# Kernel tuning notes

Hardware: AMD Instinct MI355X
Metric: run time of the kernel (lower is better)

The kernel has to match this reference:

```python
import jax, jax.numpy as jnp
import numpy as np


def _conv_relu(x, w, b):
    # keras Conv2D: NHWC input, HWIO kernel, VALID padding, stride 1, relu
    y = jax.lax.conv_general_dilated(
        x, w, window_strides=(1, 1), padding='VALID',
        dimension_numbers=('NHWC', 'HWIO', 'NHWC'))
    return jax.nn.relu(y + b)


def _maxpool2(x):
    # keras MaxPooling2D((2,2)): window 2x2, stride 2, VALID
    return jax.lax.reduce_window(
        x, -jnp.inf, jax.lax.max,
        window_dimensions=(1, 2, 2, 1), window_strides=(1, 2, 2, 1),
        padding='VALID')


def setup_inputs() -> dict:
    key = jax.random.key(0)
    ks = jax.random.split(key, 8)
    B = 4096
    return {
        'x': jax.random.normal(ks[0], (B, 14, 14, 1), jnp.float32),
        'conv1_w': jax.random.normal(ks[1], (3, 3, 1, 32), jnp.float32) * 0.1,
        'conv1_b': jnp.zeros((32,), jnp.float32),
        'conv2_w': jax.random.normal(ks[2], (3, 3, 32, 64), jnp.float32) * 0.05,
        'conv2_b': jnp.zeros((64,), jnp.float32),
        # trainable grid, initialized as tf.linspace(0,1,grid_size=50)
        'grid': jnp.linspace(0.0, 1.0, 50, dtype=jnp.float32),
        # KANLayer splines: output_dim=128 weights, each (input_dim=256, grid_size=50)
        'kan1_w': jax.random.normal(ks[3], (128, 256, 50), jnp.float32) * 0.05,
        # SimplifiedKANLayer splines: output_dim=64 weights, each (input_dim=128,)
        'kan2_w': jax.random.normal(ks[4], (64, 128), jnp.float32) * 0.05,
        'dense_w': jax.random.normal(ks[5], (64, 10), jnp.float32) * 0.05,
        'dense_b': jnp.zeros((10,), jnp.float32),
    }


def reference(x, conv1_w, conv1_b, conv2_w, conv2_b, grid, kan1_w, kan2_w,
              dense_w, dense_b):
    h = _conv_relu(x, conv1_w, conv1_b)   # (B,12,12,32)
    h = _maxpool2(h)                      # (B,6,6,32)
    h = _conv_relu(h, conv2_w, conv2_b)   # (B,4,4,64)
    h = _maxpool2(h)                      # (B,2,2,64)
    B = h.shape[0]
    h = h.reshape(B, -1)                  # (B,256) keras Flatten order (H,W,C)
    # KANLayer: linear hat basis relu(1-|x-g|) per (feature,grid), contracted
    # against per-output coefficients: out[b,o] = sum_{d,g} W[o,d,g]*basis[b,d,g]
    basis = jax.nn.relu(1.0 - jnp.abs(h[:, :, None] - grid[None, None, :]))  # (B,256,50)
    h = jnp.einsum('bdg,odg->bo', basis, kan1_w)  # (B,128)
    # SimplifiedKANLayer: out[b,o] = sum_d W2[o,d]*relu(h[b,d])
    h = jnp.einsum('bd,od->bo', jax.nn.relu(h), kan2_w)  # (B,64)
    return jax.nn.softmax(h @ dense_w + dense_b, axis=-1)  # (B,10)
```

## Files before the change

kernel.cpp:

```cpp
#include <hip/hip_runtime.h>
#include <hip/hip_bf16.h>
#include <hip/hip_fp16.h>

typedef float v2f __attribute__((ext_vector_type(2)));
typedef _Float16 f16x8 __attribute__((ext_vector_type(8)));
typedef float f32x4 __attribute__((ext_vector_type(4)));

__global__ __launch_bounds__(256) void k_prep(
    const float* __restrict__ kan1_w, const float* __restrict__ w2,
    const float* __restrict__ kan2_w, __half* __restrict__ tabN,
    _Float16* __restrict__ w2f, __half2* __restrict__ w2t) {
  int bid = blockIdx.x;
  int t = threadIdx.x;
  if (bid < 256) {
    if (t < 128) {
      int d = bid, o = t;
      const float* wp = kan1_w + (size_t)o * 12800 + (size_t)d * 50;
      float w[50];
#pragma unroll
      for (int i = 0; i < 25; ++i) {
        float2 v = *(const float2*)(wp + 2 * i);
        w[2 * i] = v.x;
        w[2 * i + 1] = v.y;
      }
      float lowW = w[0], lowG = 0.f;
      float highW = 0.f, highG = 0.f;
#pragma unroll
      for (int g = 1; g < 50; ++g) {
        highW += w[g];
        highG += w[g] * ((float)g * (1.0f / 49.0f));
      }
      __half* trow = tabN + (size_t)d * 197 * 128 + o;
      const float inv98 = 1.0f / 98.0f;
#pragma unroll
      for (int j = 0; j < 98; ++j) {
        float A = highW - lowW;
        float Bc = (lowW + highW) + lowG - highG;
        float c0 = (float)(2 * j) * inv98 + 0.5f * inv98;
        float c1 = c0 + inv98;
        trow[(size_t)(2 * j) * 128] = __float2half(fmaf(A, c0, Bc));
        trow[(size_t)(2 * j + 1) * 128] = __float2half(fmaf(A, c1, Bc));
        if (j + 1 <= 49) {
          float wg = w[j + 1], gg = (float)(j + 1) * (1.0f / 49.0f);
          lowW += wg; lowG += wg * gg;
          highW -= wg; highG -= wg * gg;
        }
        if (j >= 48) {
          float wg = w[j - 48], gg = (float)(j - 48) * (1.0f / 49.0f);
          lowW -= wg; lowG -= wg * gg;
        }
      }
      trow[(size_t)196 * 128] = __float2half(0.f);
    }
    return;
  }
  if (bid < 328) {
    int i = (bid - 256) * 256 + t;
    int n = i & 63;
    int row = i >> 6;
    int ci = row & 31;
    int tap = row >> 5;
    w2f[((tap * 4 + (ci >> 3)) * 64 + n) * 8 + (ci & 7)] = (_Float16)w2[i];
    return;
  }
  {
    int i = (bid - 328) * 256 + t;
    int dp = i >> 6;
    int o = i & 63;
    w2t[i] = __floats2half2_rn(kan2_w[o * 128 + 2 * dp],
                               kan2_w[o * 128 + 2 * dp + 1]);
  }
}

#define NBC 4

__global__ __launch_bounds__(256) void k_main(
    const float* __restrict__ x, const float* __restrict__ w1,
    const float* __restrict__ b1, const _Float16* __restrict__ w2f,
    const float* __restrict__ b2, const __half* __restrict__ tabN,
    const __half2* __restrict__ w2t, const float* __restrict__ dense_w,
    const float* __restrict__ dense_b, float* __restrict__ out) {
  __shared__ __align__(16) char sm1[4864];
  __shared__ __align__(16) char sm2[11520];
  float* xs = (float*)sm1;
  float* w1s = xs + NBC * 224;
  float* b1s = w1s + 288;
  unsigned short* meta = (unsigned short*)sm1;
  _Float16* h1l = (_Float16*)sm2;
  float* vs = (float*)sm2;
  float* us = vs + NBC * 128;
  float* ls = us + NBC * 64;
  int t = threadIdx.x;
  int bid = blockIdx.x;
  int b0 = bid * NBC;
  {
    for (int i = t; i < NBC * 224; i += 256) {
      int blb = i / 224;
      int rem = i - blb * 224;
      int r = rem >> 4;
      int cc = rem & 15;
      xs[i] = (cc < 14) ? x[(size_t)(b0 + blb) * 196 + r * 14 + cc] : 0.f;
    }
    for (int i = t; i < 288; i += 256) w1s[i] = w1[i];
    if (t < 32) b1s[t] = b1[t];
  }
  __syncthreads();
  int p = t >> 6;
  int c = t & 63;
  {
    int ch = c & 31;
    int half = c >> 5;
    float wr[9];
#pragma unroll
    for (int j = 0; j < 9; ++j) wr[j] = w1s[j * 32 + ch];
    float bias = b1s[ch];
    int y0 = 3 * half;
    const float* xb = xs + p * 224;
    _Float16* hrow = h1l + p * 1440 + ch;
#pragma unroll
    for (int yy = 0; yy < 3; ++yy) {
      int y = y0 + yy;
      float xr[4][16];
#pragma unroll
      for (int r = 0; r < 4; ++r) {
        float4* dstp = (float4*)xr[r];
        const float4* srcp = (const float4*)(xb + (2 * y + r) * 16);
#pragma unroll
        for (int q = 0; q < 4; ++q) dstp[q] = srcp[q];
      }
#pragma unroll
      for (int xx = 0; xx < 6; ++xx) {
        float m = -1e30f;
#pragma unroll
        for (int py = 0; py < 2; ++py)
#pragma unroll
          for (int px = 0; px < 2; ++px) {
            float s = 0.f;
#pragma unroll
            for (int dy = 0; dy < 3; ++dy)
#pragma unroll
              for (int dx = 0; dx < 3; ++dx)
                s = fmaf(xr[py + dy][2 * xx + px + dx], wr[dy * 3 + dx], s);
            m = fmaxf(m, s);
          }
        hrow[(y * 6 + xx) * 40] = (_Float16)fmaxf(m + bias, 0.f);
      }
    }
  }
  __syncthreads();
  {
    int lm = c & 15;
    int lk = c >> 4;
    int mbase = (lm >> 2) * 6 + (lm & 3);
    f32x4 acc[4];
#pragma unroll
    for (int nt = 0; nt < 4; ++nt) acc[nt] = (f32x4){0.f, 0.f, 0.f, 0.f};
    const _Float16* h0 = &h1l[p * 1440 + lk * 8];
#pragma unroll
    for (int tap = 0; tap < 9; ++tap) {
      int tapoff = (tap / 3) * 6 + (tap % 3);
      int po = (mbase + tapoff) * 40;
      f16x8 a0 = *(const f16x8*)(h0 + po);
      const _Float16* wb = &w2f[((tap * 4 + lk) * 64 + lm) * 8];
      f16x8 bf0 = *(const f16x8*)(wb);
      f16x8 bf1 = *(const f16x8*)(wb + 128);
      f16x8 bf2 = *(const f16x8*)(wb + 256);
      f16x8 bf3 = *(const f16x8*)(wb + 384);
      acc[0] = __builtin_amdgcn_mfma_f32_16x16x32_f16(a0, bf0, acc[0], 0, 0, 0);
      acc[1] = __builtin_amdgcn_mfma_f32_16x16x32_f16(a0, bf1, acc[1], 0, 0, 0);
      acc[2] = __builtin_amdgcn_mfma_f32_16x16x32_f16(a0, bf2, acc[2], 0, 0, 0);
      acc[3] = __builtin_amdgcn_mfma_f32_16x16x32_f16(a0, bf3, acc[3], 0, 0, 0);
    }
    float bias[4];
#pragma unroll
    for (int nt = 0; nt < 4; ++nt) bias[nt] = b2[nt * 16 + lm];
#pragma unroll
    for (int nt = 0; nt < 4; ++nt) {
      f32x4 A = acc[nt];
      float m01 = fmaxf(A.x, A.y);
      float m23 = fmaxf(A.z, A.w);
      m01 = fmaxf(m01, __shfl_xor(m01, 16));
      m23 = fmaxf(m23, __shfl_xor(m23, 16));
      float val = (lk & 1) ? m23 : m01;
      val = fmaxf(val + bias[nt], 0.f);
      int d = lk * 64 + nt * 16 + lm;
      int k = (int)(val * 98.0f);
      k = k > 196 ? 196 : k;
      meta[d * NBC + p] = (unsigned short)(d * 197 + k);
    }
  }
  __syncthreads();
  {
    int lq = c >> 4;
    int lo = c & 15;
    int phase0 = bid & 7;
    v2f acc[4];
#pragma unroll
    for (int e = 0; e < 4; ++e) acc[e] = (v2f){0.f, 0.f};
    for (int ph = 0; ph < 8; ++ph) {
      int d0 = ((phase0 + ph) & 7) << 5;
      int offs[8];
#pragma unroll
      for (int dq = 0; dq < 8; ++dq)
        offs[dq] = ((int)meta[(d0 + 4 * dq + lq) * NBC + p]) << 7;
      float4 raws[8];
#pragma unroll
      for (int dq = 0; dq < 8; ++dq)
        raws[dq] = *(const float4*)(tabN + offs[dq] + lo * 8);
#pragma unroll
      for (int dq = 0; dq < 8; ++dq) {
        float2 f0 = __half22float2(__builtin_bit_cast(__half2, raws[dq].x));
        float2 f1 = __half22float2(__builtin_bit_cast(__half2, raws[dq].y));
        float2 f2 = __half22float2(__builtin_bit_cast(__half2, raws[dq].z));
        float2 f3 = __half22float2(__builtin_bit_cast(__half2, raws[dq].w));
        acc[0] += (v2f){f0.x, f0.y};
        acc[1] += (v2f){f1.x, f1.y};
        acc[2] += (v2f){f2.x, f2.y};
        acc[3] += (v2f){f3.x, f3.y};
      }
    }
#pragma unroll
    for (int e = 0; e < 4; ++e) {
      acc[e].x += __shfl_xor(acc[e].x, 16);
      acc[e].y += __shfl_xor(acc[e].y, 16);
      acc[e].x += __shfl_xor(acc[e].x, 32);
      acc[e].y += __shfl_xor(acc[e].y, 32);
    }
    if (lq == 0) {
      float* vp = vs + p * 128 + lo * 8;
      *(float4*)vp = make_float4(fmaxf(acc[0].x, 0.f), fmaxf(acc[0].y, 0.f),
                                 fmaxf(acc[1].x, 0.f), fmaxf(acc[1].y, 0.f));
      *(float4*)(vp + 4) =
          make_float4(fmaxf(acc[2].x, 0.f), fmaxf(acc[2].y, 0.f),
                      fmaxf(acc[3].x, 0.f), fmaxf(acc[3].y, 0.f));
    }
  }
  __syncthreads();
  {
    float a = 0.f;
    const float* v0 = vs + p * 128;
#pragma unroll 8
    for (int dp = 0; dp < 64; ++dp) {
      float2 wf = __half22float2(w2t[dp * 64 + c]);
      float2 vq = *(const float2*)(v0 + 2 * dp);
      a = fmaf(wf.x, vq.x, a);
      a = fmaf(wf.y, vq.y, a);
    }
    us[p * 64 + c] = a;
  }
  __syncthreads();
  if (t < NBC * 10) {
    int b = t / 10;
    int j = t - b * 10;
    float s = dense_b[j];
    for (int k2 = 0; k2 < 64; ++k2)
      s = fmaf(us[b * 64 + k2], dense_w[k2 * 10 + j], s);
    ls[b * 12 + j] = s;
  }
  __syncthreads();
  if (t < NBC) {
    int b = t;
    float m = -1e30f;
#pragma unroll
    for (int j = 0; j < 10; ++j) m = fmaxf(m, ls[b * 12 + j]);
    float e[10];
    float sum = 0.f;
#pragma unroll
    for (int j = 0; j < 10; ++j) {
      e[j] = __expf(ls[b * 12 + j] - m);
      sum += e[j];
    }
    float inv = 1.0f / sum;
#pragma unroll
    for (int j = 0; j < 10; ++j) out[(size_t)(b0 + b) * 10 + j] = e[j] * inv;
  }
}

extern "C" void kernel_launch(void* const* d_in, const int* in_sizes, int n_in,
                              void* d_out, int out_size, void* d_ws, size_t ws_size,
                              hipStream_t stream) {
  const float* x      = (const float*)d_in[0];
  const float* w1     = (const float*)d_in[1];
  const float* b1     = (const float*)d_in[2];
  const float* w2     = (const float*)d_in[3];
  const float* b2     = (const float*)d_in[4];
  const float* kan1_w = (const float*)d_in[6];
  const float* kan2_w = (const float*)d_in[7];
  const float* dw     = (const float*)d_in[8];
  const float* db     = (const float*)d_in[9];
  float* out = (float*)d_out;
  int B = in_sizes[0] / 196;

  char* wsb = (char*)d_ws;
  __half* tabN = (__half*)wsb;
  size_t off1 = (size_t)256 * 197 * 128 * sizeof(__half);
  off1 = (off1 + 255) & ~(size_t)255;
  _Float16* w2f = (_Float16*)(wsb + off1);
  size_t off2 = off1 + 18432 * sizeof(_Float16);
  off2 = (off2 + 255) & ~(size_t)255;
  __half2* w2t = (__half2*)(wsb + off2);

  k_prep<<<dim3(344), dim3(256), 0, stream>>>(kan1_w, w2, kan2_w, tabN, w2f, w2t);
  k_main<<<dim3(B / NBC), dim3(256), 0, stream>>>(
      x, w1, b1, w2f, b2, tabN, w2t, dw, db, out);
}
```

Baseline: 112.5 us.

## Double main kernel threads and split prep table build across all threads

k_main now runs 512 threads per block. The extra four waves split the conv1 output columns and the KAN gather over the feature dimension, then combine their partial sums in the second KAN layer. k_prep stages kan1_w rows through shared memory and splits the 98-step table build between two thread halves, so all 256 threads work instead of 128. The aim is more waves in flight to hide gather latency, paid for with extra LDS traffic, partial-sum merging, and conv2 running on only half the waves.

```diff
diff --git a/kernel.cpp b/kernel.cpp
--- a/kernel.cpp
+++ b/kernel.cpp
@@ -10,48 +10,57 @@
     const float* __restrict__ kan1_w, const float* __restrict__ w2,
     const float* __restrict__ kan2_w, __half* __restrict__ tabN,
     _Float16* __restrict__ w2f, __half2* __restrict__ w2t) {
+  __shared__ float wsh[128][51];
   int bid = blockIdx.x;
   int t = threadIdx.x;
   if (bid < 256) {
-    if (t < 128) {
-      int d = bid, o = t;
-      const float* wp = kan1_w + (size_t)o * 12800 + (size_t)d * 50;
-      float w[50];
-#pragma unroll
-      for (int i = 0; i < 25; ++i) {
-        float2 v = *(const float2*)(wp + 2 * i);
-        w[2 * i] = v.x;
-        w[2 * i + 1] = v.y;
-      }
-      float lowW = w[0], lowG = 0.f;
-      float highW = 0.f, highG = 0.f;
-#pragma unroll
+    int d = bid;
+    for (int i = t; i < 128 * 50; i += 256) {
+      int oo = i / 50;
+      int g = i - oo * 50;
+      wsh[oo][g] = kan1_w[(size_t)oo * 12800 + (size_t)d * 50 + g];
+    }
+    __syncthreads();
+    int o = t & 127;
+    int jh = t >> 7;
+    const float* wr = &wsh[o][0];
+    __half* trow = tabN + (size_t)d * 197 * 128 + o;
+    const float inv98 = 1.0f / 98.0f;
+    float lowW, lowG, highW, highG;
+    int k0, k1;
+    if (jh == 0) {
+      lowW = wr[0]; lowG = 0.f; highW = 0.f; highG = 0.f;
       for (int g = 1; g < 50; ++g) {
-        highW += w[g];
-        highG += w[g] * ((float)g * (1.0f / 49.0f));
-      }
-      __half* trow = tabN + (size_t)d * 197 * 128 + o;
-      const float inv98 = 1.0f / 98.0f;
-#pragma unroll
-      for (int j = 0; j < 98; ++j) {
-        float A = highW - lowW;
-        float Bc = (lowW + highW) + lowG - highG;
-        float c0 = (float)(2 * j) * inv98 + 0.5f * inv98;
-        float c1 = c0 + inv98;
-        trow[(size_t)(2 * j) * 128] = __float2half(fmaf(A, c0, Bc));
-        trow[(size_t)(2 * j + 1) * 128] = __float2half(fmaf(A, c1, Bc));
-        if (j + 1 <= 49) {
-          float wg = w[j + 1], gg = (float)(j + 1) * (1.0f / 49.0f);
-          lowW += wg; lowG += wg * gg;
-          highW -= wg; highG -= wg * gg;
-        }
-        if (j >= 48) {
-          float wg = w[j - 48], gg = (float)(j - 48) * (1.0f / 49.0f);
-          lowW -= wg; lowG -= wg * gg;
-        }
-      }
-      trow[(size_t)196 * 128] = __float2half(0.f);
-    }
+        highW += wr[g];
+        highG += wr[g] * ((float)g * (1.0f / 49.0f));
+      }
+      k0 = 0; k1 = 49;
+    } else {
+      lowW = 0.f; lowG = 0.f; highW = 0.f; highG = 0.f;
+      for (int g = 1; g < 50; ++g) {
+        lowW += wr[g];
+        lowG += wr[g] * ((float)g * (1.0f / 49.0f));
+      }
+      k0 = 49; k1 = 98;
+    }
+    for (int k = k0; k < k1; ++k) {
+      float A = highW - lowW;
+      float Bc = (lowW + highW) + lowG - highG;
+      float c0 = (float)(2 * k) * inv98 + 0.5f * inv98;
+      float c1 = c0 + inv98;
+      trow[(size_t)(2 * k) * 128] = __float2half(fmaf(A, c0, Bc));
+      trow[(size_t)(2 * k + 1) * 128] = __float2half(fmaf(A, c1, Bc));
+      if (k + 1 <= 49) {
+        float wg = wr[k + 1], gg = (float)(k + 1) * (1.0f / 49.0f);
+        lowW += wg; lowG += wg * gg;
+        highW -= wg; highG -= wg * gg;
+      }
+      if (k >= 48) {
+        float wg = wr[k - 48], gg = (float)(k - 48) * (1.0f / 49.0f);
+        lowW -= wg; lowG -= wg * gg;
+      }
+    }
+    if (jh == 1) trow[(size_t)196 * 128] = __float2half(0.f);
     return;
   }
   if (bid < 328) {
@@ -74,7 +83,7 @@
 
 #define NBC 4
 
-__global__ __launch_bounds__(256) void k_main(
+__global__ __launch_bounds__(512) void k_main(
     const float* __restrict__ x, const float* __restrict__ w1,
     const float* __restrict__ b1, const _Float16* __restrict__ w2f,
     const float* __restrict__ b2, const __half* __restrict__ tabN,
@@ -88,33 +97,36 @@
   unsigned short* meta = (unsigned short*)sm1;
   _Float16* h1l = (_Float16*)sm2;
   float* vs = (float*)sm2;
-  float* us = vs + NBC * 128;
-  float* ls = us + NBC * 64;
+  float* us = (float*)(sm2 + 4096);
+  float* ls = (float*)(sm2 + 6144);
   int t = threadIdx.x;
   int bid = blockIdx.x;
   int b0 = bid * NBC;
-  {
-    for (int i = t; i < NBC * 224; i += 256) {
+  int w = t >> 6;
+  int c = t & 63;
+  int p = w & 3;
+  int half = w >> 2;
+  {
+    for (int i = t; i < NBC * 224; i += 512) {
       int blb = i / 224;
       int rem = i - blb * 224;
       int r = rem >> 4;
       int cc = rem & 15;
       xs[i] = (cc < 14) ? x[(size_t)(b0 + blb) * 196 + r * 14 + cc] : 0.f;
     }
-    for (int i = t; i < 288; i += 256) w1s[i] = w1[i];
-    if (t < 32) b1s[t] = b1[t];
-  }
-  __syncthreads();
-  int p = t >> 6;
-  int c = t & 63;
+    if (t < 288) w1s[t] = w1[t];
+    else if (t < 320) b1s[t - 288] = b1[t - 288];
+  }
+  __syncthreads();
   {
     int ch = c & 31;
-    int half = c >> 5;
+    int yh = c >> 5;
     float wr[9];
 #pragma unroll
     for (int j = 0; j < 9; ++j) wr[j] = w1s[j * 32 + ch];
     float bias = b1s[ch];
-    int y0 = 3 * half;
+    int y0 = 3 * yh;
+    int x0 = 3 * half;
     const float* xb = xs + p * 224;
     _Float16* hrow = h1l + p * 1440 + ch;
 #pragma unroll
@@ -129,7 +141,8 @@
         for (int q = 0; q < 4; ++q) dstp[q] = srcp[q];
       }
 #pragma unroll
-      for (int xx = 0; xx < 6; ++xx) {
+      for (int xx = 0; xx < 3; ++xx) {
+        int xc = x0 + xx;
         float m = -1e30f;
 #pragma unroll
         for (int py = 0; py < 2; ++py)
@@ -140,15 +153,15 @@
             for (int dy = 0; dy < 3; ++dy)
 #pragma unroll
               for (int dx = 0; dx < 3; ++dx)
-                s = fmaf(xr[py + dy][2 * xx + px + dx], wr[dy * 3 + dx], s);
+                s = fmaf(xr[py + dy][2 * xc + px + dx], wr[dy * 3 + dx], s);
             m = fmaxf(m, s);
           }
-        hrow[(y * 6 + xx) * 40] = (_Float16)fmaxf(m + bias, 0.f);
-      }
-    }
-  }
-  __syncthreads();
-  {
+        hrow[(y * 6 + xc) * 40] = (_Float16)fmaxf(m + bias, 0.f);
+      }
+    }
+  }
+  __syncthreads();
+  if (half == 0) {
     int lm = c & 15;
     int lk = c >> 4;
     int mbase = (lm >> 2) * 6 + (lm & 3);
@@ -193,12 +206,13 @@
   {
     int lq = c >> 4;
     int lo = c & 15;
-    int phase0 = bid & 7;
+    int dbase = half << 7;
+    int phase0 = bid & 3;
     v2f acc[4];
 #pragma unroll
     for (int e = 0; e < 4; ++e) acc[e] = (v2f){0.f, 0.f};
-    for (int ph = 0; ph < 8; ++ph) {
-      int d0 = ((phase0 + ph) & 7) << 5;
+    for (int ph = 0; ph < 4; ++ph) {
+      int d0 = dbase + (((phase0 + ph) & 3) << 5);
       int offs[8];
 #pragma unroll
       for (int dq = 0; dq < 8; ++dq)
@@ -227,26 +241,29 @@
       acc[e].y += __shfl_xor(acc[e].y, 32);
     }
     if (lq == 0) {
-      float* vp = vs + p * 128 + lo * 8;
-      *(float4*)vp = make_float4(fmaxf(acc[0].x, 0.f), fmaxf(acc[0].y, 0.f),
-                                 fmaxf(acc[1].x, 0.f), fmaxf(acc[1].y, 0.f));
-      *(float4*)(vp + 4) =
-          make_float4(fmaxf(acc[2].x, 0.f), fmaxf(acc[2].y, 0.f),
-                      fmaxf(acc[3].x, 0.f), fmaxf(acc[3].y, 0.f));
+      float* vp = vs + (half * NBC + p) * 128 + lo * 8;
+      *(float4*)vp = make_float4(acc[0].x, acc[0].y, acc[1].x, acc[1].y);
+      *(float4*)(vp + 4) = make_float4(acc[2].x, acc[2].y, acc[3].x, acc[3].y);
     }
   }
   __syncthreads();
   {
     float a = 0.f;
     const float* v0 = vs + p * 128;
+    const float* v1 = vs + (NBC + p) * 128;
+    int dp0 = half * 32;
 #pragma unroll 8
-    for (int dp = 0; dp < 64; ++dp) {
+    for (int dpi = 0; dpi < 32; ++dpi) {
+      int dp = dp0 + dpi;
       float2 wf = __half22float2(w2t[dp * 64 + c]);
-      float2 vq = *(const float2*)(v0 + 2 * dp);
-      a = fmaf(wf.x, vq.x, a);
-      a = fmaf(wf.y, vq.y, a);
-    }
-    us[p * 64 + c] = a;
+      float2 qa = *(const float2*)(v0 + 2 * dp);
+      float2 qb = *(const float2*)(v1 + 2 * dp);
+      float vx = fmaxf(qa.x + qb.x, 0.f);
+      float vy = fmaxf(qa.y + qb.y, 0.f);
+      a = fmaf(wf.x, vx, a);
+      a = fmaf(wf.y, vy, a);
+    }
+    us[(half * NBC + p) * 64 + c] = a;
   }
   __syncthreads();
   if (t < NBC * 10) {
@@ -254,7 +271,8 @@
     int j = t - b * 10;
     float s = dense_b[j];
     for (int k2 = 0; k2 < 64; ++k2)
-      s = fmaf(us[b * 64 + k2], dense_w[k2 * 10 + j], s);
+      s = fmaf(us[b * 64 + k2] + us[(NBC + b) * 64 + k2],
+               dense_w[k2 * 10 + j], s);
     ls[b * 12 + j] = s;
   }
   __syncthreads();
@@ -301,6 +319,6 @@
   __half2* w2t = (__half2*)(wsb + off2);
 
   k_prep<<<dim3(344), dim3(256), 0, stream>>>(kan1_w, w2, kan2_w, tabN, w2f, w2t);
-  k_main<<<dim3(B / NBC), dim3(256), 0, stream>>>(
+  k_main<<<dim3(B / NBC), dim3(512), 0, stream>>>(
       x, w1, b1, w2f, b2, tabN, w2t, dw, db, out);
 }
```

Result: slower. 198.0 us (+75.9%).
